# Performance work log

Measured on AMD Instinct MI355X. Metric: run time of the kernel, lower is better.

Reference implementation:

```python
import jax, jax.numpy as jnp
import numpy as np

SHIFT_MAX = 20.0  # max |offset| in pixels; padded margin is (M-N)/2 = 32

def setup_inputs() -> dict:
    key = jax.random.key(0)
    k1, k2 = jax.random.split(key)
    B, M, N, C = 2048, 128, 64, 4
    padded_obj = jax.random.normal(k1, (B, M, M, 1), dtype=jnp.float32)
    # channel-format offsets (B,1,2,C): [...,0,:] = x (col) shift, [...,1,:] = y (row) shift
    positions = (jax.random.uniform(k2, (B, 1, 2, C), dtype=jnp.float32) - 0.5) * 2.0 * SHIFT_MAX
    return {"padded_obj": padded_obj, "positions": positions, "N": N}


def _bilinear_extract(padded_obj, positions, N):
    # padded_obj: (B,M,M,1), positions: (B,1,2,C) -> patches (B,N,N,C)
    # Equivalent to: translate each (per-channel) copy of the object by -offset
    # with bilinear interpolation and zero fill, then crop the central NxN.
    B, M = padded_obj.shape[0], padded_obj.shape[1]
    C = positions.shape[-1]
    img = padded_obj[..., 0]                       # (B,M,M)
    ox = positions[:, 0, 0, :]                     # (B,C) x (column) offset
    oy = positions[:, 0, 1, :]                     # (B,C) y (row) offset
    c0 = (M - N) // 2                              # crop origin
    r = jnp.arange(N, dtype=positions.dtype)
    # sample coordinates in source image: out(r,c) = img(r + c0 + oy, c + c0 + ox)
    yy = r[None, None, :] + c0 + oy[..., None]     # (B,C,N)
    xx = r[None, None, :] + c0 + ox[..., None]     # (B,C,N)
    y0 = jnp.floor(yy)
    x0 = jnp.floor(xx)
    wy = (yy - y0)[:, :, :, None]                  # (B,C,N,1) row frac
    wx = (xx - x0)[:, :, None, :]                  # (B,C,1,N) col frac
    y0i = y0.astype(jnp.int32)
    x0i = x0.astype(jnp.int32)
    b_idx = jnp.arange(B)[:, None, None, None]

    def gather(yi, xi):
        # yi: (B,C,N) rows, xi: (B,C,N) cols -> (B,C,N,N) with zero fill OOB
        valid = ((yi[:, :, :, None] >= 0) & (yi[:, :, :, None] < M)
                 & (xi[:, :, None, :] >= 0) & (xi[:, :, None, :] < M))
        yc = jnp.clip(yi, 0, M - 1)[:, :, :, None]
        xc = jnp.clip(xi, 0, M - 1)[:, :, None, :]
        vals = img[b_idx, yc, xc]                  # (B,C,N,N)
        return jnp.where(valid, vals, jnp.zeros((), vals.dtype))

    v00 = gather(y0i, x0i)
    v01 = gather(y0i, x0i + 1)
    v10 = gather(y0i + 1, x0i)
    v11 = gather(y0i + 1, x0i + 1)
    patch = (v00 * (1 - wy) * (1 - wx) + v01 * (1 - wy) * wx
             + v10 * wy * (1 - wx) + v11 * wy * wx)   # (B,C,N,N)
    return jnp.transpose(patch, (0, 2, 3, 1))          # (B,N,N,C)


def reference(padded_obj, positions, N):
    return _bilinear_extract(padded_obj, positions, N)
```

## Files before the change

### kernel.cpp

```cpp
#include <hip/hip_runtime.h>


constexpr int Mdim   = 128;
constexpr int Npatch = 64;
constexpr int Cc     = 4;
constexpr int C0     = 32;
constexpr int ROW0   = 12;
constexpr int NROWS  = 104;

__global__ __launch_bounds__(512) void extract_patches_kernel(
    const float* __restrict__ img,
    const float* __restrict__ pos,
    float* __restrict__ out)
{
    __shared__ float lds[NROWS * Mdim];

    const int b = blockIdx.x;
    const float* __restrict__ imgb = img + (size_t)b * (Mdim * Mdim);
    const float* __restrict__ pb   = pos + (size_t)b * (2 * Cc);

    const int tid  = threadIdx.x;
    const int lane = tid & 63;
    const int wave = tid >> 6;

    const float* src = imgb + ROW0 * Mdim;
    for (int w = wave; w < (NROWS * Mdim) / 256; w += 8) {
        const float* g = src + w * 256 + lane * 4;
        __builtin_amdgcn_global_load_lds(
            (const __attribute__((address_space(1))) void*)g,
            (__attribute__((address_space(3))) void*)&lds[w * 256],
            16, 0, 0);
    }

    float w00[Cc], w01[Cc], w10[Cc], w11[Cc];
    int   base0[Cc];
#pragma unroll
    for (int c = 0; c < Cc; ++c) {
        const float ox = pb[c];
        const float oy = pb[Cc + c];
        const float fx = floorf(ox);
        const float fy = floorf(oy);
        const float wx = ox - fx;
        const float wy = oy - fy;
        const int ix = C0 + (int)fx;
        const int iy = C0 + (int)fy;
        base0[c] = (iy - ROW0) * Mdim + ix;
        w00[c] = (1.0f - wy) * (1.0f - wx);
        w01[c] = (1.0f - wy) * wx;
        w10[c] = wy * (1.0f - wx);
        w11[c] = wy * wx;
    }

    __syncthreads();

    const int j  = tid & (Npatch - 1);
    const int i0 = tid >> 6;

    for (int i = i0; i < Npatch; i += 8) {
        float4 o;
        float* res = reinterpret_cast<float*>(&o);
#pragma unroll
        for (int c = 0; c < Cc; ++c) {
            const int base = base0[c] + i * Mdim + j;
            const float v00 = lds[base];
            const float v01 = lds[base + 1];
            const float v10 = lds[base + Mdim];
            const float v11 = lds[base + Mdim + 1];
            res[c] = w00[c] * v00 + w01[c] * v01 + w10[c] * v10 + w11[c] * v11;
        }
        float4* optr = reinterpret_cast<float4*>(
            out + (((size_t)b * Npatch + i) * Npatch + j) * Cc);
        *optr = o;
    }
}

extern "C" void kernel_launch(void* const* d_in, const int* in_sizes, int n_in,
                              void* d_out, int out_size, void* d_ws, size_t ws_size,
                              hipStream_t stream) {
    const float* img = (const float*)d_in[0];
    const float* pos = (const float*)d_in[1];
    float* out = (float*)d_out;

    const int B = in_sizes[0] / (Mdim * Mdim);
    extract_patches_kernel<<<dim3(B), dim3(512), 0, stream>>>(img, pos, out);
}
```

Measured before the change: 232.4 us.

## Split each image across two blocks and reuse rows along vertical sweeps

Each image is now handled by two blocks, each producing 32 output rows. A block stages only the 74 source rows its half needs, starting at a data-dependent row. Each thread computes 4 consecutive output rows and carries the lower interpolation row forward in registers, so each new row needs only two LDS reads per channel. The smaller LDS footprint and the occupancy hint in launch bounds aim to fit more blocks per CU and hide latency. The cost is overlapping global reads between the two halves of an image and somewhat more per-block setup.

```diff
diff --git a/kernel.cpp b/kernel.cpp
--- a/kernel.cpp
+++ b/kernel.cpp
@@ -5,17 +5,18 @@
 constexpr int Npatch = 64;
 constexpr int Cc     = 4;
 constexpr int C0     = 32;
-constexpr int ROW0   = 12;
-constexpr int NROWS  = 104;
+constexpr int SROWS  = 74;
 
-__global__ __launch_bounds__(512) void extract_patches_kernel(
+__global__ __launch_bounds__(512, 8) void extract_patches_kernel(
     const float* __restrict__ img,
     const float* __restrict__ pos,
     float* __restrict__ out)
 {
-    __shared__ float lds[NROWS * Mdim];
+    __shared__ float lds[SROWS * Mdim];
 
-    const int b = blockIdx.x;
+    const int bid  = blockIdx.x;
+    const int b    = bid >> 1;
+    const int h    = bid & 1;
     const float* __restrict__ imgb = img + (size_t)b * (Mdim * Mdim);
     const float* __restrict__ pb   = pos + (size_t)b * (2 * Cc);
 
@@ -23,17 +24,8 @@
     const int lane = tid & 63;
     const int wave = tid >> 6;
 
-    const float* src = imgb + ROW0 * Mdim;
-    for (int w = wave; w < (NROWS * Mdim) / 256; w += 8) {
-        const float* g = src + w * 256 + lane * 4;
-        __builtin_amdgcn_global_load_lds(
-            (const __attribute__((address_space(1))) void*)g,
-            (__attribute__((address_space(3))) void*)&lds[w * 256],
-            16, 0, 0);
-    }
-
     float w00[Cc], w01[Cc], w10[Cc], w11[Cc];
-    int   base0[Cc];
+    int   iyv[Cc], ixv[Cc];
 #pragma unroll
     for (int c = 0; c < Cc; ++c) {
         const float ox = pb[c];
@@ -42,35 +34,56 @@
         const float fy = floorf(oy);
         const float wx = ox - fx;
         const float wy = oy - fy;
-        const int ix = C0 + (int)fx;
-        const int iy = C0 + (int)fy;
-        base0[c] = (iy - ROW0) * Mdim + ix;
+        ixv[c] = C0 + (int)fx;
+        iyv[c] = C0 + (int)fy;
         w00[c] = (1.0f - wy) * (1.0f - wx);
         w01[c] = (1.0f - wy) * wx;
         w10[c] = wy * (1.0f - wx);
         w11[c] = wy * wx;
     }
 
+    int min_iy = min(min(iyv[0], iyv[1]), min(iyv[2], iyv[3]));
+    int r0 = min(min_iy + 32 * h, Mdim - SROWS);
+
+    const float* src = imgb + r0 * Mdim;
+    for (int w = wave; w < (SROWS * Mdim) / 256; w += 8) {
+        const float* g = src + w * 256 + lane * 4;
+        __builtin_amdgcn_global_load_lds(
+            (const __attribute__((address_space(1))) void*)g,
+            (__attribute__((address_space(3))) void*)&lds[w * 256],
+            16, 0, 0);
+    }
+
     __syncthreads();
 
-    const int j  = tid & (Npatch - 1);
-    const int i0 = tid >> 6;
+    const int j   = tid & 63;
+    const int s   = tid >> 6;
+    const int li0 = s * 4;
 
-    for (int i = i0; i < Npatch; i += 8) {
+    int   a[Cc];
+    float p0[Cc], p1[Cc];
+#pragma unroll
+    for (int c = 0; c < Cc; ++c) {
+        a[c] = (iyv[c] + 32 * h + li0 - r0) * Mdim + ixv[c] + j;
+        p0[c] = lds[a[c]];
+        p1[c] = lds[a[c] + 1];
+    }
+
+    float* obase = out + (((size_t)b * Npatch + 32 * h + li0) * Npatch + j) * Cc;
+#pragma unroll
+    for (int k = 0; k < 4; ++k) {
         float4 o;
         float* res = reinterpret_cast<float*>(&o);
 #pragma unroll
         for (int c = 0; c < Cc; ++c) {
-            const int base = base0[c] + i * Mdim + j;
-            const float v00 = lds[base];
-            const float v01 = lds[base + 1];
-            const float v10 = lds[base + Mdim];
-            const float v11 = lds[base + Mdim + 1];
-            res[c] = w00[c] * v00 + w01[c] * v01 + w10[c] * v10 + w11[c] * v11;
+            a[c] += Mdim;
+            const float n0 = lds[a[c]];
+            const float n1 = lds[a[c] + 1];
+            res[c] = w00[c] * p0[c] + w01[c] * p1[c] + w10[c] * n0 + w11[c] * n1;
+            p0[c] = n0;
+            p1[c] = n1;
         }
-        float4* optr = reinterpret_cast<float4*>(
-            out + (((size_t)b * Npatch + i) * Npatch + j) * Cc);
-        *optr = o;
+        *reinterpret_cast<float4*>(obase + (size_t)k * Npatch * Cc) = o;
     }
 }
 
@@ -82,5 +95,5 @@
     float* out = (float*)d_out;
 
     const int B = in_sizes[0] / (Mdim * Mdim);
-    extract_patches_kernel<<<dim3(B), dim3(512), 0, stream>>>(img, pos, out);
+    extract_patches_kernel<<<dim3(2 * B), dim3(512), 0, stream>>>(img, pos, out);
 }
```

After: 231.8 us. No clear change (-0.3%).
